# Optimization experiments

Hardware: AMD Instinct MI355X
Metric: run time of the kernel (lower is better)

The kernel has to match this reference:

```python
import jax, jax.numpy as jnp
import numpy as np

B, S, E, H = 8, 512, 1024, 16
Dh = E // H
MAX_LEN = 512


def setup_inputs() -> dict:
    key = jax.random.key(0)
    ks = jax.random.split(key, 16)
    std = 1.0 / np.sqrt(E)
    inp = {
        "query": jax.random.normal(ks[0], (B, S, E), jnp.float32),
        "key": jax.random.normal(ks[1], (B, S, E), jnp.float32),
        "value": jax.random.normal(ks[2], (B, S, E), jnp.float32),
        "Wq": jax.random.normal(ks[3], (E, E), jnp.float32) * std,
        "bq": jax.random.normal(ks[4], (E,), jnp.float32) * std,
        "Wk": jax.random.normal(ks[5], (E, E), jnp.float32) * std,
        "bk": jax.random.normal(ks[6], (E,), jnp.float32) * std,
        "Wv": jax.random.normal(ks[7], (E, E), jnp.float32) * std,
        "bv": jax.random.normal(ks[8], (E,), jnp.float32) * std,
        "Wo": jax.random.normal(ks[9], (E, E), jnp.float32) * std,
        "bo": jax.random.normal(ks[10], (E,), jnp.float32) * std,
        "pos": jax.random.normal(ks[11], (MAX_LEN, 1, E), jnp.float32),
    }
    return inp


def reference(query, key, value, Wq, bq, Wk, bk, Wv, bv, Wo, bo, pos):
    b, sq, e = query.shape
    s = min(sq, key.shape[1])  # target_seq_length (static)
    scale = np.sqrt(Dh).astype(np.float32)
    pe = pos[:s, 0, :][None]  # [1, s, E] broadcast over batch
    q = query[:, :s] @ Wq.T + bq + pe
    k = key[:, :s] @ Wk.T + bk + pe
    v = value[:, :s] @ Wv.T + bv + pe
    # [b, s, H, Dh]
    q = q.reshape(b, s, H, Dh)
    k = k.reshape(b, s, H, Dh)
    v = v.reshape(b, s, H, Dh)
    scores = jnp.einsum("bqhd,bkhd->bhqk", q, k) / scale
    attn = jax.nn.softmax(scores, axis=-1)
    wv = jnp.einsum("bhqk,bkhd->bqhd", attn, v).reshape(b, s, e)
    return wv @ Wo.T + bo
```

## Files before the change

kernel.cpp:

```cpp
#include <hip/hip_runtime.h>
#include <hip/hip_bf16.h>

typedef __attribute__((ext_vector_type(8))) short bfx8;
typedef __attribute__((ext_vector_type(4))) short bfx4;
typedef __attribute__((ext_vector_type(4))) float fx4;

static __device__ __forceinline__ short f2bf(float f) {
  union { float f; unsigned u; } v; v.f = f;
  unsigned r = v.u + 0x7fffu + ((v.u >> 16) & 1u);
  return (short)(r >> 16);
}

static __device__ __forceinline__ void gld16(const void* g, void* l) {
  __builtin_amdgcn_global_load_lds(
      (const __attribute__((address_space(1))) void*)g,
      (__attribute__((address_space(3))) void*)l, 16, 0, 0);
}

constexpr int Bz = 8, Sq = 512, Em = 1024, Hn = 16, Dh = 64;
constexpr int Mrows = Bz * Sq;
constexpr size_t NE = (size_t)Mrows * Em;
constexpr size_t WE = (size_t)Em * Em;

__global__ __launch_bounds__(256) void convert_kernel(
    const float* __restrict__ q, const float* __restrict__ k,
    const float* __restrict__ v,
    const float* __restrict__ Wq, const float* __restrict__ Wk,
    const float* __restrict__ Wv, const float* __restrict__ Wo,
    short* __restrict__ qx, short* __restrict__ kx, short* __restrict__ vx,
    short* __restrict__ wqb, short* __restrict__ wkb,
    short* __restrict__ wvb, short* __restrict__ wob)
{
  const size_t c = (size_t)blockIdx.x * 256 + threadIdx.x;
  constexpr size_t CI = NE / 8;
  constexpr size_t CW = WE / 8;
  const float* src; short* dst; size_t off;
  if (c < 3 * CI) {
    const int sgi = (int)(c / CI);
    src = sgi == 0 ? q : sgi == 1 ? k : v;
    dst = sgi == 0 ? qx : sgi == 1 ? kx : vx;
    off = (c - (size_t)sgi * CI) * 8;
  } else {
    const size_t w = c - 3 * CI;
    const int sgi = (int)(w / CW);
    src = sgi == 0 ? Wq : sgi == 1 ? Wk : sgi == 2 ? Wv : Wo;
    dst = sgi == 0 ? wqb : sgi == 1 ? wkb : sgi == 2 ? wvb : wob;
    off = (w - (size_t)sgi * CW) * 8;
  }
  fx4 a = *(const fx4*)(src + off);
  fx4 b = *(const fx4*)(src + off + 4);
  bfx8 o = { f2bf(a[0]), f2bf(a[1]), f2bf(a[2]), f2bf(a[3]),
             f2bf(b[0]), f2bf(b[1]), f2bf(b[2]), f2bf(b[3]) };
  *(bfx8*)(dst + off) = o;
}

constexpr int LDP = 136;

__global__ __launch_bounds__(256, 4) void gemm_qkv_bf16(
    const short* __restrict__ qx, const short* __restrict__ kx,
    const short* __restrict__ vx,
    const short* __restrict__ Wqb, const short* __restrict__ Wkb,
    const short* __restrict__ Wvb,
    const float* __restrict__ bq, const float* __restrict__ bk,
    const float* __restrict__ bv,
    const float* __restrict__ pos,
    short* __restrict__ qb, short* __restrict__ kb, short* __restrict__ vb)
{
  __shared__ short SM[128 * LDP];
  short* As = SM;
  short* Bs = SM + 8192;

  const int z = blockIdx.z;
  const short* X = (z == 0) ? qx : (z == 1) ? kx : vx;
  const short* W = (z == 0) ? Wqb : (z == 1) ? Wkb : Wvb;
  const float* bias = (z == 0) ? bq : (z == 1) ? bk : bv;
  short* dst = (z == 0) ? qb : (z == 1) ? kb : vb;

  const int m0 = blockIdx.x * 128;
  const int n0 = blockIdx.y * 128;
  const int t = threadIdx.x, lane = t & 63, wave = t >> 6;
  const int wr = wave >> 1, wc = wave & 1;
  const int fr = lane & 15, fq = lane >> 4;

  const int trow = t >> 3;
  const int scol = ((t & 7) ^ (trow & 7)) * 8;
  const short* gW = W + (size_t)(n0 + trow) * Em + scol;
  const short* gX = X + (size_t)(m0 + trow) * Em + scol;
  short* lA = As + wave * 512;
  short* lB = Bs + wave * 512;

  const int sw0 = ((fq ^ (fr & 7)) * 8);
  const int sw1 = (((4 + fq) ^ (fr & 7)) * 8);

  fx4 acc[4][4] = {};

  for (int k0 = 0; k0 < Em; k0 += 64) {
#pragma unroll
    for (int r = 0; r < 4; ++r) {
      gld16(gW + (size_t)(32 * r) * Em + k0, lA + r * 2048);
      gld16(gX + (size_t)(32 * r) * Em + k0, lB + r * 2048);
    }
    __syncthreads();

#pragma unroll
    for (int ks = 0; ks < 2; ++ks) {
      const int sw = ks ? sw1 : sw0;
      bfx8 af[4], bf[4];
#pragma unroll
      for (int u = 0; u < 4; ++u)
        af[u] = *(const bfx8*)&As[(wr * 64 + u * 16 + fr) * 64 + sw];
#pragma unroll
      for (int v = 0; v < 4; ++v)
        bf[v] = *(const bfx8*)&Bs[(wc * 64 + v * 16 + fr) * 64 + sw];
#pragma unroll
      for (int u = 0; u < 4; ++u)
#pragma unroll
        for (int v = 0; v < 4; ++v)
          acc[u][v] = __builtin_amdgcn_mfma_f32_16x16x32_bf16(af[u], bf[v], acc[u][v], 0, 0, 0);
    }
    __syncthreads();
  }

  const int rr = t >> 4, jj = t & 15;
  const int b = m0 >> 9;
  if (z < 2) {
#pragma unroll
    for (int u = 0; u < 4; ++u) {
      const int nn = wr * 64 + u * 16 + fq * 4;
      const int nng = n0 + nn;
      const fx4 bb = *(const fx4*)&bias[nng];
#pragma unroll
      for (int v = 0; v < 4; ++v) {
        const int m = wc * 64 + v * 16 + fr;
        const int s = (m0 + m) & (Sq - 1);
        const fx4 pe = *(const fx4*)&pos[(size_t)s * Em + nng];
        const fx4 a = acc[u][v];
        bfx4 o = { f2bf(a[0] + bb[0] + pe[0]), f2bf(a[1] + bb[1] + pe[1]),
                   f2bf(a[2] + bb[2] + pe[2]), f2bf(a[3] + bb[3] + pe[3]) };
        *(bfx4*)&SM[m * LDP + nn] = o;
      }
    }
    __syncthreads();
#pragma unroll
    for (int it = 0; it < 8; ++it) {
      const int m = it * 16 + rr;
      const int s = (m0 + m) & (Sq - 1);
      bfx8 val = *(const bfx8*)&SM[m * LDP + jj * 8];
      const int nng = n0 + jj * 8;
      const int h = nng >> 6, d = nng & 63;
      *(bfx8*)&dst[(((size_t)b * Hn + h) * Sq + s) * Dh + d] = val;
    }
  } else {
#pragma unroll
    for (int u = 0; u < 4; ++u) {
      const int nnb = wr * 64 + u * 16 + fq * 4;
      const int nng = n0 + nnb;
      const fx4 bb = *(const fx4*)&bias[nng];
#pragma unroll
      for (int v = 0; v < 4; ++v) {
        const int m = wc * 64 + v * 16 + fr;
        const int s = (m0 + m) & (Sq - 1);
        const fx4 pe = *(const fx4*)&pos[(size_t)s * Em + nng];
        const fx4 a = acc[u][v];
#pragma unroll
        for (int i = 0; i < 4; ++i) {
          const int row = nnb + i;
          SM[row * LDP + (m ^ ((row & 12) << 2))] = f2bf(a[i] + bb[i] + pe[i]);
        }
      }
    }
    __syncthreads();
    const int s0 = m0 & (Sq - 1);
#pragma unroll
    for (int it = 0; it < 8; ++it) {
      const int row = it * 16 + rr;
      bfx8 val = *(const bfx8*)&SM[row * LDP + ((jj * 8) ^ ((row & 12) << 2))];
      const int nng = n0 + row;
      const int h = nng >> 6, d = nng & 63;
      *(bfx8*)&dst[(((size_t)b * Hn + h) * Dh + d) * Sq + s0 + jj * 8] = val;
    }
  }
}

__global__ __launch_bounds__(256, 4) void gemm_out_bf16(
    const short* __restrict__ wv, const short* __restrict__ Wob,
    const float* __restrict__ bo, float* __restrict__ out)
{
  __shared__ short SM[2 * 8192];
  short* As = SM;
  short* Bs = SM + 8192;

  const int m0 = blockIdx.x * 128;
  const int n0 = blockIdx.y * 128;
  const int t = threadIdx.x, lane = t & 63, wave = t >> 6;
  const int wr = wave >> 1, wc = wave & 1;
  const int fr = lane & 15, fq = lane >> 4;

  const int trow = t >> 3;
  const int scol = ((t & 7) ^ (trow & 7)) * 8;
  const short* gW = Wob + (size_t)(n0 + trow) * Em + scol;
  const short* gX = wv + (size_t)(m0 + trow) * Em + scol;
  short* lA = As + wave * 512;
  short* lB = Bs + wave * 512;

  const int sw0 = ((fq ^ (fr & 7)) * 8);
  const int sw1 = (((4 + fq) ^ (fr & 7)) * 8);

  fx4 acc[4][4] = {};

  for (int k0 = 0; k0 < Em; k0 += 64) {
#pragma unroll
    for (int r = 0; r < 4; ++r) {
      gld16(gW + (size_t)(32 * r) * Em + k0, lA + r * 2048);
      gld16(gX + (size_t)(32 * r) * Em + k0, lB + r * 2048);
    }
    __syncthreads();

#pragma unroll
    for (int ks = 0; ks < 2; ++ks) {
      const int sw = ks ? sw1 : sw0;
      bfx8 af[4], bf[4];
#pragma unroll
      for (int u = 0; u < 4; ++u)
        af[u] = *(const bfx8*)&As[(wr * 64 + u * 16 + fr) * 64 + sw];
#pragma unroll
      for (int v = 0; v < 4; ++v)
        bf[v] = *(const bfx8*)&Bs[(wc * 64 + v * 16 + fr) * 64 + sw];
#pragma unroll
      for (int u = 0; u < 4; ++u)
#pragma unroll
        for (int v = 0; v < 4; ++v)
          acc[u][v] = __builtin_amdgcn_mfma_f32_16x16x32_bf16(af[u], bf[v], acc[u][v], 0, 0, 0);
    }
    __syncthreads();
  }

#pragma unroll
  for (int u = 0; u < 4; ++u) {
    const int nn = n0 + wr * 64 + u * 16 + fq * 4;
    const fx4 bb = *(const fx4*)&bo[nn];
#pragma unroll
    for (int v = 0; v < 4; ++v) {
      const int m = m0 + wc * 64 + v * 16 + fr;
      fx4 val = acc[u][v];
      val[0] += bb[0]; val[1] += bb[1]; val[2] += bb[2]; val[3] += bb[3];
      *(fx4*)&out[(size_t)m * Em + nn] = val;
    }
  }
}

constexpr int KVB = 64, LDK = 72;

__global__ __launch_bounds__(256) void attn_kernel(
    const short* __restrict__ qb, const short* __restrict__ kb,
    const short* __restrict__ vb, short* __restrict__ wv)
{
  __shared__ short Ks[KVB * LDK];
  __shared__ short Vt[Dh * LDK];
  __shared__ short Ps[4][16 * LDK];

  const int bh = blockIdx.x;
  const int qt = blockIdx.y;
  const int t = threadIdx.x, lane = t & 63, wave = t >> 6;
  const int fr = lane & 15, fq = lane >> 4;

  const size_t base = (size_t)bh * Sq * Dh;
  const int q0 = qt * 64 + wave * 16;

  bfx8 qf[2];
  {
    const short* qp = qb + base + (size_t)(q0 + fr) * Dh;
    qf[0] = *(const bfx8*)(qp + fq * 8);
    qf[1] = *(const bfx8*)(qp + 32 + fq * 8);
  }

  float mrow[4] = { -1e30f, -1e30f, -1e30f, -1e30f };
  float lrow[4] = { 0.f, 0.f, 0.f, 0.f };
  fx4 oacc[4] = {};

  const int kr = t >> 2, kc = (t & 3) * 16;

  for (int kv0 = 0; kv0 < Sq; kv0 += KVB) {
    {
      const short* kp = kb + base + (size_t)(kv0 + kr) * Dh + kc;
      bfx8 u0 = *(const bfx8*)kp;
      bfx8 u1 = *(const bfx8*)(kp + 8);
      *(bfx8*)&Ks[kr * LDK + kc] = u0;
      *(bfx8*)&Ks[kr * LDK + kc + 8] = u1;
    }
    {
      const short* vp = vb + base + (size_t)kr * Sq + kv0 + kc;
      bfx8 u0 = *(const bfx8*)vp;
      bfx8 u1 = *(const bfx8*)(vp + 8);
      *(bfx8*)&Vt[kr * LDK + kc] = u0;
      *(bfx8*)&Vt[kr * LDK + kc + 8] = u1;
    }
    __syncthreads();

    fx4 sa[4] = {};
#pragma unroll
    for (int nf = 0; nf < 4; ++nf) {
#pragma unroll
      for (int ks = 0; ks < 2; ++ks) {
        bfx8 kf = *(const bfx8*)&Ks[(nf * 16 + fr) * LDK + ks * 32 + fq * 8];
        sa[nf] = __builtin_amdgcn_mfma_f32_16x16x32_bf16(qf[ks], kf, sa[nf], 0, 0, 0);
      }
    }

#pragma unroll
    for (int i = 0; i < 4; ++i) {
      float mx = fmaxf(fmaxf(sa[0][i], sa[1][i]), fmaxf(sa[2][i], sa[3][i]));
      mx = fmaxf(mx, __shfl_xor(mx, 1));
      mx = fmaxf(mx, __shfl_xor(mx, 2));
      mx = fmaxf(mx, __shfl_xor(mx, 4));
      mx = fmaxf(mx, __shfl_xor(mx, 8));
      mx *= 0.125f;
      const float mn = fmaxf(mrow[i], mx);
      const float alpha = __expf(mrow[i] - mn);
      mrow[i] = mn;
      float rs = 0.f;
#pragma unroll
      for (int nf = 0; nf < 4; ++nf) {
        const float p = __expf(sa[nf][i] * 0.125f - mn);
        rs += p;
        Ps[wave][(fq * 4 + i) * LDK + nf * 16 + fr] = f2bf(p);
      }
      rs += __shfl_xor(rs, 1);
      rs += __shfl_xor(rs, 2);
      rs += __shfl_xor(rs, 4);
      rs += __shfl_xor(rs, 8);
      lrow[i] = lrow[i] * alpha + rs;
#pragma unroll
      for (int df = 0; df < 4; ++df) oacc[df][i] *= alpha;
    }
    __syncthreads();

    bfx8 pf[2];
    pf[0] = *(const bfx8*)&Ps[wave][fr * LDK + fq * 8];
    pf[1] = *(const bfx8*)&Ps[wave][fr * LDK + 32 + fq * 8];
#pragma unroll
    for (int df = 0; df < 4; ++df) {
#pragma unroll
      for (int ks = 0; ks < 2; ++ks) {
        bfx8 vf = *(const bfx8*)&Vt[(df * 16 + fr) * LDK + ks * 32 + fq * 8];
        oacc[df] = __builtin_amdgcn_mfma_f32_16x16x32_bf16(pf[ks], vf, oacc[df], 0, 0, 0);
      }
    }
    __syncthreads();
  }

  const int b = bh >> 4, h = bh & 15;
#pragma unroll
  for (int df = 0; df < 4; ++df) {
    const int d = df * 16 + fr;
#pragma unroll
    for (int i = 0; i < 4; ++i) {
      const int qrow = q0 + fq * 4 + i;
      const float o = oacc[df][i] / lrow[i];
      wv[((size_t)b * Sq + qrow) * Em + h * Dh + d] = f2bf(o);
    }
  }
}

extern "C" void kernel_launch(void* const* d_in, const int* in_sizes, int n_in,
                              void* d_out, int out_size, void* d_ws, size_t ws_size,
                              hipStream_t stream) {
  (void)in_sizes; (void)n_in; (void)out_size; (void)ws_size;
  const float* query = (const float*)d_in[0];
  const float* key   = (const float*)d_in[1];
  const float* value = (const float*)d_in[2];
  const float* Wq = (const float*)d_in[3];
  const float* bq = (const float*)d_in[4];
  const float* Wk = (const float*)d_in[5];
  const float* bk = (const float*)d_in[6];
  const float* Wv = (const float*)d_in[7];
  const float* bv = (const float*)d_in[8];
  const float* Wo = (const float*)d_in[9];
  const float* bo = (const float*)d_in[10];
  const float* pos = (const float*)d_in[11];

  short* qx = (short*)d_ws;
  short* kx = qx + NE;
  short* vx = kx + NE;
  short* Wqb = vx + NE;
  short* Wkb = Wqb + WE;
  short* Wvb = Wkb + WE;
  short* Wob = Wvb + WE;
  short* qb = Wob + WE;
  short* wv = qx;
  short* kb = (short*)d_out;
  short* vb = kb + NE;

  convert_kernel<<<dim3(8192), 256, 0, stream>>>(
      query, key, value, Wq, Wk, Wv, Wo, qx, kx, vx, Wqb, Wkb, Wvb, Wob);
  gemm_qkv_bf16<<<dim3(Mrows / 128, Em / 128, 3), 256, 0, stream>>>(
      qx, kx, vx, Wqb, Wkb, Wvb, bq, bk, bv, pos, qb, kb, vb);
  attn_kernel<<<dim3(Bz * Hn, Sq / 64), 256, 0, stream>>>(qb, kb, vb, wv);
  gemm_out_bf16<<<dim3(Mrows / 128, Em / 128), 256, 0, stream>>>(
      wv, Wob, bo, (float*)d_out);
}
```

Measured before the change: 116.4 us.

## Prefetch next K/V tile into registers during attention compute

In the flash-attention kernel, the global loads for the next K and V tile now go into registers while the current tile's QK^T, softmax and PV MFMAs run. The registers are stored to LDS after the post-PV barrier. The barrier between writing P and reading it back is removed, since each wave only touches its own Ps slice. The aim is to hide global-load latency behind compute and cut one block-wide sync per iteration, at the cost of extra VGPRs for the prefetched fragments.

```diff
diff --git a/kernel.cpp b/kernel.cpp
--- a/kernel.cpp
+++ b/kernel.cpp
@@ -274,28 +274,37 @@
     qf[1] = *(const bfx8*)(qp + 32 + fq * 8);
   }
 
+  const int kr = t >> 2, kc = (t & 3) * 16;
+  const short* kbp = kb + base + (size_t)kr * Dh + kc;
+  const short* vbp = vb + base + (size_t)kr * Sq + kc;
+
+  {
+    bfx8 k0 = *(const bfx8*)kbp;
+    bfx8 k1 = *(const bfx8*)(kbp + 8);
+    bfx8 v0 = *(const bfx8*)vbp;
+    bfx8 v1 = *(const bfx8*)(vbp + 8);
+    *(bfx8*)&Ks[kr * LDK + kc] = k0;
+    *(bfx8*)&Ks[kr * LDK + kc + 8] = k1;
+    *(bfx8*)&Vt[kr * LDK + kc] = v0;
+    *(bfx8*)&Vt[kr * LDK + kc + 8] = v1;
+  }
+  __syncthreads();
+
   float mrow[4] = { -1e30f, -1e30f, -1e30f, -1e30f };
   float lrow[4] = { 0.f, 0.f, 0.f, 0.f };
   fx4 oacc[4] = {};
 
-  const int kr = t >> 2, kc = (t & 3) * 16;
-
   for (int kv0 = 0; kv0 < Sq; kv0 += KVB) {
-    {
-      const short* kp = kb + base + (size_t)(kv0 + kr) * Dh + kc;
-      bfx8 u0 = *(const bfx8*)kp;
-      bfx8 u1 = *(const bfx8*)(kp + 8);
-      *(bfx8*)&Ks[kr * LDK + kc] = u0;
-      *(bfx8*)&Ks[kr * LDK + kc + 8] = u1;
-    }
-    {
-      const short* vp = vb + base + (size_t)kr * Sq + kv0 + kc;
-      bfx8 u0 = *(const bfx8*)vp;
-      bfx8 u1 = *(const bfx8*)(vp + 8);
-      *(bfx8*)&Vt[kr * LDK + kc] = u0;
-      *(bfx8*)&Vt[kr * LDK + kc + 8] = u1;
-    }
-    __syncthreads();
+    const bool more = (kv0 + KVB) < Sq;
+    bfx8 nk0, nk1, nv0, nv1;
+    if (more) {
+      const short* nk = kbp + (size_t)(kv0 + KVB) * Dh;
+      const short* nv = vbp + (kv0 + KVB);
+      nk0 = *(const bfx8*)nk;
+      nk1 = *(const bfx8*)(nk + 8);
+      nv0 = *(const bfx8*)nv;
+      nv1 = *(const bfx8*)(nv + 8);
+    }
 
     fx4 sa[4] = {};
 #pragma unroll
@@ -333,7 +342,6 @@
 #pragma unroll
       for (int df = 0; df < 4; ++df) oacc[df][i] *= alpha;
     }
-    __syncthreads();
 
     bfx8 pf[2];
     pf[0] = *(const bfx8*)&Ps[wave][fr * LDK + fq * 8];
@@ -347,6 +355,14 @@
       }
     }
     __syncthreads();
+
+    if (more) {
+      *(bfx8*)&Ks[kr * LDK + kc] = nk0;
+      *(bfx8*)&Ks[kr * LDK + kc + 8] = nk1;
+      *(bfx8*)&Vt[kr * LDK + kc] = nv0;
+      *(bfx8*)&Vt[kr * LDK + kc + 8] = nv1;
+      __syncthreads();
+    }
   }
 
   const int b = bh >> 4, h = bh & 15;
```

Result: no change. 115.7 us (-0.7%).
